# Kernel optimization log

Hardware: AMD Instinct MI355X
Metric: run time of the kernel (lower is better)

## Reference

```python
import jax, jax.numpy as jnp
import numpy as np

V = 100000   # vocab_size
H = 128      # hidden_dim
B = 4096     # number of sentences in the batch
T = 409600


def setup_inputs() -> dict:
    key = jax.random.key(0)
    k_tok, k_seg, k_y, k_e, k_wh, k_bh, k_wo, k_bo = jax.random.split(key, 8)
    token_ids = jax.random.randint(k_tok, (T,), 0, V, dtype=jnp.int32)
    segment_ids = jnp.sort(jax.random.randint(k_seg, (T,), 0, B, dtype=jnp.int32))
    y_true = jax.random.uniform(k_y, (B,), dtype=jnp.float32)
    # learned parameters (nn.Embedding ~ N(0,1); Linear ~ U(-1/sqrt(fan_in), +))
    embed_table = jax.random.normal(k_e, (V, H), dtype=jnp.float32)
    lim = 1.0 / np.sqrt(H)
    W_hid = jax.random.uniform(k_wh, (H, H), minval=-lim, maxval=lim, dtype=jnp.float32)
    b_hid = jax.random.uniform(k_bh, (H,), minval=-lim, maxval=lim, dtype=jnp.float32)
    W_out = jax.random.uniform(k_wo, (H, 1), minval=-lim, maxval=lim, dtype=jnp.float32)
    b_out = jax.random.uniform(k_bo, (1,), minval=-lim, maxval=lim, dtype=jnp.float32)
    return {
        "token_ids": token_ids,
        "segment_ids": segment_ids,
        "y_true": y_true,
        "embed_table": embed_table,
        "W_hid": W_hid,
        "b_hid": b_hid,
        "W_out": W_out,
        "b_out": b_out,
    }


def reference(token_ids, segment_ids, y_true, embed_table, W_hid, b_hid, W_out, b_out):
    # Fused gather + segment-mean (replaces the per-sentence Python loop).
    tok_emb = embed_table[token_ids]                                    # [T, H]
    sums = jax.ops.segment_sum(tok_emb, segment_ids, num_segments=B)   # [B, H]
    counts = jax.ops.segment_sum(jnp.ones((T,), tok_emb.dtype), segment_ids,
                                 num_segments=B)                        # [B]
    sent_embeds = sums / jnp.maximum(counts, 1.0)[:, None]             # [B, H]
    # Small MLP head: tanh hidden -> sigmoid scalar score.
    hid = jnp.tanh(sent_embeds @ W_hid + b_hid)                        # [B, H]
    probas = jax.nn.sigmoid(hid @ W_out + b_out).squeeze(-1)           # [B]
    # BCE with size_average=False (sum reduction); torch clamps log at -100.
    log_p = jnp.clip(jnp.log(probas), -100.0)
    log_1mp = jnp.clip(jnp.log1p(-probas), -100.0)
    total_loss = -jnp.sum(y_true * log_p + (1.0 - y_true) * log_1mp)
    return total_loss
```

## Files before the change

### kernel.cpp

```cpp
#include <hip/hip_runtime.h>
#include <math.h>

#define HDIM 128

__global__ void init_kernel(int* __restrict__ starts, int nB1, int Tval,
                            float* __restrict__ out) {
    int i = blockIdx.x * blockDim.x + threadIdx.x;
    if (i < nB1) starts[i] = Tval;
    if (i == 0) out[0] = 0.0f;
}

__global__ void seg_bounds_kernel(const int* __restrict__ seg,
                                  int* __restrict__ starts, int Tval) {
    int t = blockIdx.x * blockDim.x + threadIdx.x;
    if (t >= Tval) return;
    int b = seg[t];
    int a = (t == 0) ? -1 : seg[t - 1];
    for (int s = a + 1; s <= b; ++s) starts[s] = t;
}

__global__ __launch_bounds__(256) void gather_mean_kernel(
    const int* __restrict__ tok, const float* __restrict__ emb,
    const int* __restrict__ starts, float* __restrict__ sent, int Bval) {
    int wave = threadIdx.x >> 6;
    int lane = threadIdx.x & 63;
    int s = blockIdx.x * 4 + wave;
    if (s >= Bval) return;

    int t0 = starts[s];
    int t1 = starts[s + 1];
    int cnt = t1 - t0;

    int half = lane >> 5;
    int col  = lane & 31;

    float4 acc = make_float4(0.f, 0.f, 0.f, 0.f);

    int i = t0 + half;
    for (; i + 6 < t1; i += 8) {
        int ta = tok[i];
        int tb = tok[i + 2];
        int tc = tok[i + 4];
        int td = tok[i + 6];
        float4 fa = ((const float4*)(emb + (size_t)ta * HDIM))[col];
        float4 fb = ((const float4*)(emb + (size_t)tb * HDIM))[col];
        float4 fc = ((const float4*)(emb + (size_t)tc * HDIM))[col];
        float4 fd = ((const float4*)(emb + (size_t)td * HDIM))[col];
        acc.x += fa.x + fb.x + fc.x + fd.x;
        acc.y += fa.y + fb.y + fc.y + fd.y;
        acc.z += fa.z + fb.z + fc.z + fd.z;
        acc.w += fa.w + fb.w + fc.w + fd.w;
    }
    for (; i < t1; i += 2) {
        int ta = tok[i];
        float4 fa = ((const float4*)(emb + (size_t)ta * HDIM))[col];
        acc.x += fa.x; acc.y += fa.y; acc.z += fa.z; acc.w += fa.w;
    }

    acc.x += __shfl_down(acc.x, 32);
    acc.y += __shfl_down(acc.y, 32);
    acc.z += __shfl_down(acc.z, 32);
    acc.w += __shfl_down(acc.w, 32);

    if (half == 0) {
        float inv = 1.0f / (float)(cnt > 0 ? cnt : 1);
        acc.x *= inv; acc.y *= inv; acc.z *= inv; acc.w *= inv;
        ((float4*)(sent + (size_t)s * HDIM))[col] = acc;
    }
}

__global__ __launch_bounds__(256) void mlp_loss_kernel(
    const float* __restrict__ sent, const float* __restrict__ Wh,
    const float* __restrict__ bh, const float* __restrict__ Wo,
    const float* __restrict__ bo, const float* __restrict__ y,
    float* __restrict__ out, int Bval, int nblocks) {
    __shared__ float Wlds[HDIM * HDIM];
    __shared__ float slds[4][4 * HDIM];
    __shared__ float lred[4];

    for (int idx = threadIdx.x; idx < HDIM * HDIM / 4; idx += 256)
        ((float4*)Wlds)[idx] = ((const float4*)Wh)[idx];
    __syncthreads();

    int wave = threadIdx.x >> 6;
    int lane = threadIdx.x & 63;
    int j0 = lane * 2;

    float bh0 = bh[j0], bh1 = bh[j0 + 1];
    float wo0 = Wo[j0], wo1 = Wo[j0 + 1];
    float bov = bo[0];
    float lsum = 0.0f;

    const float2* W2 = (const float2*)Wlds;
    float* myld = &slds[wave][0];

    for (int base0 = blockIdx.x * 16; base0 < Bval; base0 += nblocks * 16) {
        int base = base0 + wave * 4;
        int rem = Bval - base;
        int nseg = rem < 4 ? (rem < 0 ? 0 : rem) : 4;

        for (int r = 0; r < nseg; ++r) {
            float2 v = ((const float2*)(sent + (size_t)(base + r) * HDIM))[lane];
            ((float2*)(myld + r * HDIM))[lane] = v;
        }

        float a00 = bh0, a01 = bh1, a10 = bh0, a11 = bh1;
        float a20 = bh0, a21 = bh1, a30 = bh0, a31 = bh1;
        for (int i = 0; i < HDIM; ++i) {
            float2 w = W2[i * (HDIM / 2) + lane];
            float s0 = myld[0 * HDIM + i];
            float s1 = myld[1 * HDIM + i];
            float s2 = myld[2 * HDIM + i];
            float s3 = myld[3 * HDIM + i];
            a00 = fmaf(s0, w.x, a00); a01 = fmaf(s0, w.y, a01);
            a10 = fmaf(s1, w.x, a10); a11 = fmaf(s1, w.y, a11);
            a20 = fmaf(s2, w.x, a20); a21 = fmaf(s2, w.y, a21);
            a30 = fmaf(s3, w.x, a30); a31 = fmaf(s3, w.y, a31);
        }

        float pr0 = tanhf(a00) * wo0 + tanhf(a01) * wo1;
        float pr1 = tanhf(a10) * wo0 + tanhf(a11) * wo1;
        float pr2 = tanhf(a20) * wo0 + tanhf(a21) * wo1;
        float pr3 = tanhf(a30) * wo0 + tanhf(a31) * wo1;
        for (int m = 1; m < 64; m <<= 1) {
            pr0 += __shfl_xor(pr0, m);
            pr1 += __shfl_xor(pr1, m);
            pr2 += __shfl_xor(pr2, m);
            pr3 += __shfl_xor(pr3, m);
        }

        if (lane == 0) {
            float prs[4] = {pr0, pr1, pr2, pr3};
            for (int r = 0; r < nseg; ++r) {
                float z = prs[r] + bov;
                float p = 1.0f / (1.0f + expf(-z));
                float lp  = fmaxf(logf(p),     -100.0f);
                float l1p = fmaxf(log1pf(-p),  -100.0f);
                float yv = y[base + r];
                lsum -= yv * lp + (1.0f - yv) * l1p;
            }
        }
    }

    if (lane == 0) lred[wave] = lsum;
    __syncthreads();
    if (threadIdx.x == 0) {
        float tot = lred[0] + lred[1] + lred[2] + lred[3];
        atomicAdd(out, tot);
    }
}

extern "C" void kernel_launch(void* const* d_in, const int* in_sizes, int n_in,
                              void* d_out, int out_size, void* d_ws, size_t ws_size,
                              hipStream_t stream) {
    const int*   tok = (const int*)d_in[0];
    const int*   seg = (const int*)d_in[1];
    const float* y   = (const float*)d_in[2];
    const float* emb = (const float*)d_in[3];
    const float* Wh  = (const float*)d_in[4];
    const float* bh  = (const float*)d_in[5];
    const float* Wo  = (const float*)d_in[6];
    const float* bo  = (const float*)d_in[7];

    int T_ = in_sizes[0];
    int B_ = in_sizes[2];

    float* out = (float*)d_out;

    int* starts = (int*)d_ws;
    size_t starts_bytes = ((size_t)(B_ + 1) * sizeof(int) + 255) & ~(size_t)255;
    float* sent = (float*)((char*)d_ws + starts_bytes);

    init_kernel<<<(B_ + 1 + 255) / 256, 256, 0, stream>>>(starts, B_ + 1, T_, out);
    seg_bounds_kernel<<<(T_ + 255) / 256, 256, 0, stream>>>(seg, starts, T_);
    gather_mean_kernel<<<(B_ + 3) / 4, 256, 0, stream>>>(tok, emb, starts, sent, B_);
    int nblocks = (B_ + 15) / 16;
    if (nblocks > 256) nblocks = 256;
    mlp_loss_kernel<<<nblocks, 256, 0, stream>>>(sent, Wh, bh, Wo, bo, y, out, B_, nblocks);
}
```

Baseline: 136.5 us.

## Drop init kernel, split each segment over two waves, prefetch token ids

```diff
diff --git a/kernel.cpp b/kernel.cpp
--- a/kernel.cpp
+++ b/kernel.cpp
@@ -3,29 +3,31 @@
 
 #define HDIM 128
 
-__global__ void init_kernel(int* __restrict__ starts, int nB1, int Tval,
-                            float* __restrict__ out) {
-    int i = blockIdx.x * blockDim.x + threadIdx.x;
-    if (i < nB1) starts[i] = Tval;
-    if (i == 0) out[0] = 0.0f;
-}
-
-__global__ void seg_bounds_kernel(const int* __restrict__ seg,
-                                  int* __restrict__ starts, int Tval) {
+__global__ __launch_bounds__(256) void seg_bounds_kernel(
+    const int* __restrict__ seg, int* __restrict__ starts,
+    int Tval, int Bval, float* __restrict__ out) {
     int t = blockIdx.x * blockDim.x + threadIdx.x;
     if (t >= Tval) return;
     int b = seg[t];
     int a = (t == 0) ? -1 : seg[t - 1];
     for (int s = a + 1; s <= b; ++s) starts[s] = t;
+    if (t == Tval - 1) {
+        for (int s = b + 1; s <= Bval; ++s) starts[s] = Tval;
+    }
+    if (t == 0) out[0] = 0.0f;
 }
 
 __global__ __launch_bounds__(256) void gather_mean_kernel(
     const int* __restrict__ tok, const float* __restrict__ emb,
     const int* __restrict__ starts, float* __restrict__ sent, int Bval) {
+    __shared__ float4 part[2][32];
+
     int wave = threadIdx.x >> 6;
     int lane = threadIdx.x & 63;
-    int s = blockIdx.x * 4 + wave;
-    if (s >= Bval) return;
+    int segslot = wave >> 1;
+    int parity  = wave & 1;
+    int s = blockIdx.x * 2 + segslot;
+    if (s >= Bval) s = Bval - 1;
 
     int t0 = starts[s];
     int t1 = starts[s + 1];
@@ -33,36 +35,47 @@
 
     int half = lane >> 5;
     int col  = lane & 31;
+    int q = parity * 2 + half;
 
     float4 acc = make_float4(0.f, 0.f, 0.f, 0.f);
 
-    int i = t0 + half;
-    for (; i + 6 < t1; i += 8) {
-        int ta = tok[i];
-        int tb = tok[i + 2];
-        int tc = tok[i + 4];
-        int td = tok[i + 6];
-        float4 fa = ((const float4*)(emb + (size_t)ta * HDIM))[col];
-        float4 fb = ((const float4*)(emb + (size_t)tb * HDIM))[col];
-        float4 fc = ((const float4*)(emb + (size_t)tc * HDIM))[col];
-        float4 fd = ((const float4*)(emb + (size_t)td * HDIM))[col];
-        acc.x += fa.x + fb.x + fc.x + fd.x;
-        acc.y += fa.y + fb.y + fc.y + fd.y;
-        acc.z += fa.z + fb.z + fc.z + fd.z;
-        acc.w += fa.w + fb.w + fc.w + fd.w;
+    int i = t0 + q;
+    if (i + 12 < t1) {
+        int ta = tok[i], tb = tok[i + 4], tc = tok[i + 8], td = tok[i + 12];
+        for (;;) {
+            float4 fa = ((const float4*)(emb + (size_t)ta * HDIM))[col];
+            float4 fb = ((const float4*)(emb + (size_t)tb * HDIM))[col];
+            float4 fc = ((const float4*)(emb + (size_t)tc * HDIM))[col];
+            float4 fd = ((const float4*)(emb + (size_t)td * HDIM))[col];
+            int ni = i + 16;
+            bool more = (ni + 12 < t1);
+            if (more) {
+                ta = tok[ni]; tb = tok[ni + 4]; tc = tok[ni + 8]; td = tok[ni + 12];
+            }
+            acc.x += fa.x + fb.x + fc.x + fd.x;
+            acc.y += fa.y + fb.y + fc.y + fd.y;
+            acc.z += fa.z + fb.z + fc.z + fd.z;
+            acc.w += fa.w + fb.w + fc.w + fd.w;
+            i = ni;
+            if (!more) break;
+        }
     }
-    for (; i < t1; i += 2) {
-        int ta = tok[i];
-        float4 fa = ((const float4*)(emb + (size_t)ta * HDIM))[col];
-        acc.x += fa.x; acc.y += fa.y; acc.z += fa.z; acc.w += fa.w;
+    for (; i < t1; i += 4) {
+        int tt = tok[i];
+        float4 f = ((const float4*)(emb + (size_t)tt * HDIM))[col];
+        acc.x += f.x; acc.y += f.y; acc.z += f.z; acc.w += f.w;
     }
 
-    acc.x += __shfl_down(acc.x, 32);
-    acc.y += __shfl_down(acc.y, 32);
-    acc.z += __shfl_down(acc.z, 32);
-    acc.w += __shfl_down(acc.w, 32);
+    acc.x += __shfl_xor(acc.x, 32);
+    acc.y += __shfl_xor(acc.y, 32);
+    acc.z += __shfl_xor(acc.z, 32);
+    acc.w += __shfl_xor(acc.w, 32);
 
-    if (half == 0) {
+    if (parity == 1 && half == 0) part[segslot][col] = acc;
+    __syncthreads();
+    if (parity == 0 && half == 0) {
+        float4 o = part[segslot][col];
+        acc.x += o.x; acc.y += o.y; acc.z += o.z; acc.w += o.w;
         float inv = 1.0f / (float)(cnt > 0 ? cnt : 1);
         acc.x *= inv; acc.y *= inv; acc.z *= inv; acc.w *= inv;
         ((float4*)(sent + (size_t)s * HDIM))[col] = acc;
@@ -171,9 +184,8 @@
     size_t starts_bytes = ((size_t)(B_ + 1) * sizeof(int) + 255) & ~(size_t)255;
     float* sent = (float*)((char*)d_ws + starts_bytes);
 
-    init_kernel<<<(B_ + 1 + 255) / 256, 256, 0, stream>>>(starts, B_ + 1, T_, out);
-    seg_bounds_kernel<<<(T_ + 255) / 256, 256, 0, stream>>>(seg, starts, T_);
-    gather_mean_kernel<<<(B_ + 3) / 4, 256, 0, stream>>>(tok, emb, starts, sent, B_);
+    seg_bounds_kernel<<<(T_ + 255) / 256, 256, 0, stream>>>(seg, starts, T_, B_, out);
+    gather_mean_kernel<<<(B_ + 1) / 2, 256, 0, stream>>>(tok, emb, starts, sent, B_);
     int nblocks = (B_ + 15) / 16;
     if (nblocks > 256) nblocks = 256;
     mlp_loss_kernel<<<nblocks, 256, 0, stream>>>(sent, Wh, bh, Wo, bo, y, out, B_, nblocks);
```

Measured after the change: 137.2 us. No clear change (+0.5%).
